# Kernel optimization log

Measured on AMD Instinct MI355X. Metric: run time of the kernel, lower is better.

Reference implementation:

```python
import jax, jax.numpy as jnp
import numpy as np

K_DIM = 1024
HEADS = 16
D_K = K_DIM // HEADS


def setup_inputs() -> dict:
    key = jax.random.key(0)
    ks = jax.random.split(key, 6)
    b, t, k = 4, 1024, K_DIM
    scale = 1.0 / np.sqrt(k)
    return {
        "x": jax.random.normal(ks[0], (b, t, k), dtype=jnp.float32),
        "Wq": jax.random.normal(ks[1], (k, k), dtype=jnp.float32) * scale,
        "Wk": jax.random.normal(ks[2], (k, k), dtype=jnp.float32) * scale,
        "Wv": jax.random.normal(ks[3], (k, k), dtype=jnp.float32) * scale,
        "Wo": jax.random.normal(ks[4], (k, k), dtype=jnp.float32) * scale,
        "bo": jax.random.normal(ks[5], (k,), dtype=jnp.float32) * 0.01,
    }


def reference(x, Wq, Wk, Wv, Wo, bo):
    b, t, k = x.shape
    h, d_k = HEADS, D_K
    # Linear(k,k) applies x @ W.T; project then split heads -> [b, h, t, d_k]
    Q = (x @ Wq.T).reshape(b, t, h, d_k).transpose(0, 2, 1, 3)
    Kh = (x @ Wk.T).reshape(b, t, h, d_k).transpose(0, 2, 1, 3)
    V = (x @ Wv.T).reshape(b, t, h, d_k).transpose(0, 2, 1, 3)
    scores = jnp.einsum("bhqd,bhkd->bhqk", Q, Kh) / jnp.sqrt(jnp.float32(d_k))
    attn = jax.nn.softmax(scores, axis=-1)
    out = jnp.einsum("bhqk,bhkd->bhqd", attn, V)
    out = out.transpose(0, 2, 1, 3).reshape(b, t, k)
    return out @ Wo.T + bo
```

## Files before the change

kernel.cpp:

```cpp
#include <hip/hip_runtime.h>
#include <hip/hip_bf16.h>

typedef __attribute__((ext_vector_type(4))) float f32x4;
typedef __attribute__((ext_vector_type(8))) short short8;

#define B_   4
#define T_   1024
#define H_   16
#define DK_  64
#define KDIM 1024

#define QSCALE 0.18033688011112042f

__device__ __forceinline__ unsigned short f2bf(float f){
  union { float f; unsigned int u; } a; a.f = f;
  unsigned int u = a.u;
  return (unsigned short)((u + 0x7FFFu + ((u >> 16) & 1u)) >> 16);
}

__device__ __forceinline__ unsigned short f2bf_rn(float f){
  union { __hip_bfloat16 h; unsigned short u; } cv;
  cv.h = __float2bfloat16(f);
  return cv.u;
}

__device__ __forceinline__ void gload16(const void* g, void* l){
  __builtin_amdgcn_global_load_lds(
      (const __attribute__((address_space(1))) unsigned int*)g,
      (__attribute__((address_space(3))) unsigned int*)l,
      16, 0, 0);
}

template<int N> __device__ __forceinline__ void wait_vmcnt(){
  if constexpr (N == 0)      asm volatile("s_waitcnt vmcnt(0)" ::: "memory");
  else if constexpr (N == 4) asm volatile("s_waitcnt vmcnt(4)" ::: "memory");
  else if constexpr (N == 6) asm volatile("s_waitcnt vmcnt(6)" ::: "memory");
}

__global__ __launch_bounds__(256) void convert5(
    const float* __restrict__ x,  const float* __restrict__ wq,
    const float* __restrict__ wk, const float* __restrict__ wv,
    const float* __restrict__ wo,
    short* __restrict__ xb,  short* __restrict__ wqb,
    short* __restrict__ wkb, short* __restrict__ wvb, short* __restrict__ wob)
{
  int i = blockIdx.x * 256 + threadIdx.x;
  const float* s; short* d; int off;
  if (i < (1 << 20)) { s = x; d = xb; off = i; }
  else {
    int j = i - (1 << 20);
    int w = j >> 18;
    off = j & ((1 << 18) - 1);
    s = (w == 0) ? wq : (w == 1) ? wk : (w == 2) ? wv : wo;
    d = (w == 0) ? wqb : (w == 1) ? wkb : (w == 2) ? wvb : wob;
  }
  float4 v = ((const float4*)s)[off];
  ushort4 o;
  o.x = f2bf(v.x); o.y = f2bf(v.y); o.z = f2bf(v.z); o.w = f2bf(v.w);
  ((ushort4*)d)[off] = o;
}

template<int BM, int BN>
__device__ __forceinline__ void stage_range(
    const short* __restrict__ A, const short* __restrict__ W,
    int m0, int n0, int kt, int lo, int hi,
    short* Asb, short* Bsb, int wv, int lane)
{
  constexpr int LA = BM / 64, LB = BN / 64;
  const int r8 = lane >> 3;
  const int c8 = ((lane & 7) * 8) ^ (r8 * 8);
#pragma unroll
  for (int i = lo; i < hi; ++i) {
    if (i < LA) {
      const int r = (wv * LA + i) * 8 + r8;
      gload16(A + (size_t)(m0 + r) * KDIM + kt * 64 + c8, Asb + (wv * LA + i) * 512);
    } else {
      const int ib = i - LA;
      const int r = (wv * LB + ib) * 8 + r8;
      gload16(W + (size_t)(n0 + r) * KDIM + kt * 64 + c8, Bsb + (wv * LB + ib) * 512);
    }
  }
}

template<int BM, int BN>
__device__ __forceinline__ void gemm8_core(
    const short* __restrict__ A, const short* __restrict__ W,
    int m0, int n0, short* As, short* Bs,
    f32x4 acc[BM / 64][BN / 32])
{
  constexpr int M_REP = BM / 64, N_REP = BN / 32;
  constexpr int LA = BM / 64, LB = BN / 64, L = LA + LB;
  constexpr int NKT = 16;
  const int tid = threadIdx.x;
  const int wv = tid >> 6, lane = tid & 63;
  const int lr = lane & 15, lq = lane >> 4;
  const int wm = wv >> 1, wn = wv & 1;
  const int arow = wm * (BM / 4);
  const int brow = wn * (BN / 2);
  const int swz = (lr & 7) << 3;

#pragma unroll
  for (int m = 0; m < M_REP; ++m)
#pragma unroll
    for (int n = 0; n < N_REP; ++n) acc[m][n] = (f32x4){0.f, 0.f, 0.f, 0.f};

  stage_range<BM, BN>(A, W, m0, n0, 0, 0, L, As,           Bs,           wv, lane);
  stage_range<BM, BN>(A, W, m0, n0, 1, 0, L, As + BM * 64, Bs + BN * 64, wv, lane);

  int buf = 0;
  for (int kt = 0; kt < NKT; ++kt) {
    if (kt < NKT - 1) wait_vmcnt<L>(); else wait_vmcnt<0>();
    __builtin_amdgcn_s_barrier();
    const short* Ab = As + buf * (BM * 64);
    const short* Bb = Bs + buf * (BN * 64);
    const int sb = (buf >= 1) ? buf - 1 : 2;
    short* Asb = As + sb * (BM * 64);
    short* Bsb = Bs + sb * (BN * 64);
#pragma unroll
    for (int kk = 0; kk < 2; ++kk) {
      short8 af[M_REP], bfv[N_REP];
#pragma unroll
      for (int m = 0; m < M_REP; ++m)
        af[m] = *(const short8*)(Ab + (arow + m * 16 + lr) * 64 + ((kk * 32 + lq * 8) ^ swz));
#pragma unroll
      for (int n = 0; n < N_REP; ++n)
        bfv[n] = *(const short8*)(Bb + (brow + n * 16 + lr) * 64 + ((kk * 32 + lq * 8) ^ swz));
      if (kt + 2 < NKT)
        stage_range<BM, BN>(A, W, m0, n0, kt + 2, kk * (L / 2), (kk + 1) * (L / 2),
                            Asb, Bsb, wv, lane);
      __builtin_amdgcn_s_barrier();
      __builtin_amdgcn_s_setprio(1);
#pragma unroll
      for (int m = 0; m < M_REP; ++m)
#pragma unroll
        for (int n = 0; n < N_REP; ++n)
          acc[m][n] = __builtin_amdgcn_mfma_f32_16x16x32_bf16(af[m], bfv[n], acc[m][n], 0, 0, 0);
      __builtin_amdgcn_s_setprio(0);
      __builtin_amdgcn_sched_barrier(0);
      __builtin_amdgcn_s_barrier();
    }
    buf = (buf == 2) ? 0 : buf + 1;
  }
}

__global__ __launch_bounds__(512, 2) void gemm8_qkv(
    const short* __restrict__ xb,
    const short* __restrict__ Wqb, const short* __restrict__ Wkb, const short* __restrict__ Wvb,
    short* __restrict__ Qb, short* __restrict__ Kb, short* __restrict__ VTb)
{
  __shared__ __align__(16) short As[3 * 256 * 64];
  __shared__ __align__(16) short Bs[3 * 128 * 64];
  const int bid = blockIdx.x;
  const int wgid = (bid & 7) * 48 + (bid >> 3);
  const int mx = wgid / 24, nyy = wgid % 24;
  const int wsel = nyy >> 3;
  const int m0 = mx * 256, n0 = (nyy & 7) * 128;
  const short* W = (wsel == 0) ? Wqb : (wsel == 1) ? Wkb : Wvb;

  f32x4 acc[4][4];
  gemm8_core<256, 128>(xb, W, m0, n0, As, Bs, acc);

  const int tid = threadIdx.x, lane = tid & 63, wv = tid >> 6;
  const int lr = lane & 15, lq = lane >> 4, wm = wv >> 1, wn = wv & 1;
  if (wsel < 2) {
    short* O = wsel ? Kb : Qb;
    const float sc = wsel ? 1.0f : QSCALE;
#pragma unroll
    for (int m = 0; m < 4; ++m)
#pragma unroll
      for (int n = 0; n < 4; ++n)
#pragma unroll
        for (int j = 0; j < 4; ++j) {
          int row = m0 + wm * 64 + m * 16 + lq * 4 + j;
          int col = n0 + wn * 64 + n * 16 + lr;
          O[(size_t)row * KDIM + col] = (short)f2bf(acc[m][n][j] * sc);
        }
  } else {
#pragma unroll
    for (int m = 0; m < 4; ++m)
#pragma unroll
      for (int n = 0; n < 4; ++n) {
        int row = m0 + wm * 64 + m * 16 + lq * 4;
        int col = n0 + wn * 64 + n * 16 + lr;
        int b = row >> 10, t = row & 1023, h = col >> 6, d = col & 63;
        ushort4 v;
        v.x = f2bf(acc[m][n][0]); v.y = f2bf(acc[m][n][1]);
        v.z = f2bf(acc[m][n][2]); v.w = f2bf(acc[m][n][3]);
        *(ushort4*)&VTb[(size_t)((b * 16 + h) * 64 + d) * 1024 + t] = v;
      }
  }
}

__global__ __launch_bounds__(512, 2) void gemm8_out(
    const short* __restrict__ AOb, const short* __restrict__ Wob,
    const float* __restrict__ bias, float* __restrict__ out)
{
  __shared__ __align__(16) short As[3 * 128 * 64];
  __shared__ __align__(16) short Bs[3 * 128 * 64];
  const int bid = blockIdx.x;
  const int wgid = (bid & 7) * 32 + (bid >> 3);
  const int mx = wgid >> 3, ny = wgid & 7;
  const int m0 = mx * 128, n0 = ny * 128;

  f32x4 acc[2][4];
  gemm8_core<128, 128>(AOb, Wob, m0, n0, As, Bs, acc);

  const int tid = threadIdx.x, lane = tid & 63, wv = tid >> 6;
  const int lr = lane & 15, lq = lane >> 4, wm = wv >> 1, wn = wv & 1;
#pragma unroll
  for (int m = 0; m < 2; ++m)
#pragma unroll
    for (int n = 0; n < 4; ++n) {
      int col = n0 + wn * 64 + n * 16 + lr;
      float bv = bias[col];
#pragma unroll
      for (int j = 0; j < 4; ++j) {
        int row = m0 + wm * 32 + m * 16 + lq * 4 + j;
        out[(size_t)row * KDIM + col] = acc[m][n][j] + bv;
      }
    }
}

__global__ __launch_bounds__(256) void attn_kern(
    const short* __restrict__ Qb, const short* __restrict__ Kb,
    const short* __restrict__ VTb, short* __restrict__ AOb)
{
  __shared__ __align__(16) short kl[2][64 * 64];
  __shared__ __align__(16) short vl[2][64 * 64];
  __shared__ __align__(16) short pl[4][16 * 64];
  const int bh = blockIdx.y, b = bh >> 4, h = bh & 15;
  const int q0 = blockIdx.x * 64;
  const int tid = threadIdx.x, wv = tid >> 6, lane = tid & 63;
  const int lr = lane & 15, lq = lane >> 4;

  const short* Qrow = Qb + (size_t)(b * T_ + q0 + wv * 16 + lr) * KDIM + h * DK_;
  short8 qf0 = *(const short8*)(Qrow + lq * 8);
  short8 qf1 = *(const short8*)(Qrow + 32 + lq * 8);

  const short* Kbase = Kb + (size_t)(b * T_) * KDIM + h * DK_;
  const short* Vbase = VTb + (size_t)(bh * DK_) * 1024;

  const int srow = tid >> 3, scol = (tid & 7) * 8;

  auto stage = [&](int buf, int kv0) {
#pragma unroll
    for (int p = 0; p < 2; ++p) {
      const int r = p * 32 + srow;
      gload16(Kbase + (size_t)(kv0 + r) * KDIM + (scol ^ ((r & 7) << 3)),
              &kl[buf][p * 2048 + wv * 512]);
    }
#pragma unroll
    for (int p = 0; p < 2; ++p) {
      const int r = p * 32 + srow;
      gload16(Vbase + (size_t)r * 1024 + kv0 + (scol ^ ((r & 7) << 3)),
              &vl[buf][p * 2048 + wv * 512]);
    }
  };

  f32x4 oacc[4];
#pragma unroll
  for (int i = 0; i < 4; ++i) oacc[i] = (f32x4){0.f, 0.f, 0.f, 0.f};
  float m_r = -1e30f, l_r = 0.f;
  const int swq = (lr & 7) << 3;
  short* plw = pl[wv];

  int cur = 0;
  stage(0, 0);
  __syncthreads();

  for (int kt = 0; kt < 16; ++kt) {
    if (kt < 15) stage(cur ^ 1, (kt + 1) * 64);

    f32x4 s[4];
#pragma unroll
    for (int nt = 0; nt < 4; ++nt) {
      const int kr = nt * 16 + lr;
      const int sw = (kr & 7) << 3;
      short8 kf0 = *(const short8*)&kl[cur][kr * 64 + ((lq * 8) ^ sw)];
      short8 kf1 = *(const short8*)&kl[cur][kr * 64 + ((32 + lq * 8) ^ sw)];
      f32x4 z = (f32x4){0.f, 0.f, 0.f, 0.f};
      z = __builtin_amdgcn_mfma_f32_16x16x32_bf16(kf0, qf0, z, 0, 0, 0);
      s[nt] = __builtin_amdgcn_mfma_f32_16x16x32_bf16(kf1, qf1, z, 0, 0, 0);
    }

    float mx;
    {
      float a0 = fmaxf(fmaxf(s[0][0], s[0][1]), fmaxf(s[0][2], s[0][3]));
      float a1 = fmaxf(fmaxf(s[1][0], s[1][1]), fmaxf(s[1][2], s[1][3]));
      float a2 = fmaxf(fmaxf(s[2][0], s[2][1]), fmaxf(s[2][2], s[2][3]));
      float a3 = fmaxf(fmaxf(s[3][0], s[3][1]), fmaxf(s[3][2], s[3][3]));
      mx = fmaxf(fmaxf(a0, a1), fmaxf(a2, a3));
    }
    mx = fmaxf(mx, __shfl_xor(mx, 16));
    mx = fmaxf(mx, __shfl_xor(mx, 32));
    if (!__all(mx <= m_r + 8.f)) {
      const float mn = fmaxf(m_r, mx);
      const float al = exp2f(m_r - mn);
      l_r *= al;
#pragma unroll
      for (int nt = 0; nt < 4; ++nt)
#pragma unroll
        for (int j = 0; j < 4; ++j) oacc[nt][j] *= al;
      m_r = mn;
    }
    float rs = 0.f;
#pragma unroll
    for (int nt = 0; nt < 4; ++nt)
#pragma unroll
      for (int j = 0; j < 4; ++j) {
        float e = exp2f(s[nt][j] - m_r);
        s[nt][j] = e;
        rs += e;
      }
    rs += __shfl_xor(rs, 16);
    rs += __shfl_xor(rs, 32);
    l_r += rs;

#pragma unroll
    for (int nt = 0; nt < 4; ++nt) {
      f32x4 v = s[nt];
      ushort4 u;
      u.x = f2bf_rn(v[0]); u.y = f2bf_rn(v[1]);
      u.z = f2bf_rn(v[2]); u.w = f2bf_rn(v[3]);
      *(ushort4*)&plw[lr * 64 + ((nt * 16 + lq * 4) ^ swq)] = u;
    }
    asm volatile("s_waitcnt lgkmcnt(0)" ::: "memory");
    short8 pf0 = *(const short8*)&plw[lr * 64 + ((lq * 8) ^ swq)];
    short8 pf1 = *(const short8*)&plw[lr * 64 + ((32 + lq * 8) ^ swq)];
#pragma unroll
    for (int ntd = 0; ntd < 4; ++ntd) {
      const int vr = ntd * 16 + lr;
      const int sw = (vr & 7) << 3;
      short8 vf0 = *(const short8*)&vl[cur][vr * 64 + ((lq * 8) ^ sw)];
      short8 vf1 = *(const short8*)&vl[cur][vr * 64 + ((32 + lq * 8) ^ sw)];
      oacc[ntd] = __builtin_amdgcn_mfma_f32_16x16x32_bf16(vf0, pf0, oacc[ntd], 0, 0, 0);
      oacc[ntd] = __builtin_amdgcn_mfma_f32_16x16x32_bf16(vf1, pf1, oacc[ntd], 0, 0, 0);
    }
    __syncthreads();
    cur ^= 1;
  }

  const float inv = 1.0f / l_r;
#pragma unroll
  for (int nt = 0; nt < 4; ++nt) {
    ushort4 u;
    u.x = f2bf_rn(oacc[nt][0] * inv);
    u.y = f2bf_rn(oacc[nt][1] * inv);
    u.z = f2bf_rn(oacc[nt][2] * inv);
    u.w = f2bf_rn(oacc[nt][3] * inv);
    *(ushort4*)&AOb[(size_t)(b * T_ + q0 + wv * 16 + lr) * KDIM + h * DK_ + nt * 16 + lq * 4] = u;
  }
}

extern "C" void kernel_launch(void* const* d_in, const int* in_sizes, int n_in,
                              void* d_out, int out_size, void* d_ws, size_t ws_size,
                              hipStream_t stream) {
  const float* x  = (const float*)d_in[0];
  const float* Wq = (const float*)d_in[1];
  const float* Wk = (const float*)d_in[2];
  const float* Wv = (const float*)d_in[3];
  const float* Wo = (const float*)d_in[4];
  const float* bo = (const float*)d_in[5];

  short* ws = (short*)d_ws;
  short* xb  = ws;
  short* Wqb = ws + 4194304;
  short* Wkb = ws + 5242880;
  short* Wvb = ws + 6291456;
  short* Wob = ws + 7340032;
  short* Qb  = ws + 8388608;
  short* Kb  = ws + 12582912;
  short* VTb = ws + 16777216;
  short* AOb = ws + 20971520;

  convert5<<<8192, 256, 0, stream>>>(x, Wq, Wk, Wv, Wo, xb, Wqb, Wkb, Wvb, Wob);
  gemm8_qkv<<<384, 512, 0, stream>>>(xb, Wqb, Wkb, Wvb, Qb, Kb, VTb);
  attn_kern<<<dim3(16, 64), 256, 0, stream>>>(Qb, Kb, VTb, AOb);
  gemm8_out<<<256, 512, 0, stream>>>(AOb, Wob, bo, (float*)d_out);
}
```

Baseline: 181.8 us.

## Replace 8-wave triple-buffered GEMMs with 4-wave double-buffered 128x128 tiles

```diff
diff --git a/kernel.cpp b/kernel.cpp
--- a/kernel.cpp
+++ b/kernel.cpp
@@ -29,12 +29,6 @@
       (const __attribute__((address_space(1))) unsigned int*)g,
       (__attribute__((address_space(3))) unsigned int*)l,
       16, 0, 0);
-}
-
-template<int N> __device__ __forceinline__ void wait_vmcnt(){
-  if constexpr (N == 0)      asm volatile("s_waitcnt vmcnt(0)" ::: "memory");
-  else if constexpr (N == 4) asm volatile("s_waitcnt vmcnt(4)" ::: "memory");
-  else if constexpr (N == 6) asm volatile("s_waitcnt vmcnt(6)" ::: "memory");
 }
 
 __global__ __launch_bounds__(256) void convert5(
@@ -60,108 +54,83 @@
   ((ushort4*)d)[off] = o;
 }
 
-template<int BM, int BN>
-__device__ __forceinline__ void stage_range(
+__device__ __forceinline__ void gemm2_core(
     const short* __restrict__ A, const short* __restrict__ W,
-    int m0, int n0, int kt, int lo, int hi,
-    short* Asb, short* Bsb, int wv, int lane)
-{
-  constexpr int LA = BM / 64, LB = BN / 64;
+    int m0, int n0, short* As, short* Bs, f32x4 acc[4][4])
+{
+  const int tid = threadIdx.x, wv = tid >> 6, lane = tid & 63;
+  const int lr = lane & 15, lq = lane >> 4;
+  const int wr = wv >> 1, wc = wv & 1;
+  const int swz = (lr & 7) << 3;
   const int r8 = lane >> 3;
   const int c8 = ((lane & 7) * 8) ^ (r8 * 8);
-#pragma unroll
-  for (int i = lo; i < hi; ++i) {
-    if (i < LA) {
-      const int r = (wv * LA + i) * 8 + r8;
-      gload16(A + (size_t)(m0 + r) * KDIM + kt * 64 + c8, Asb + (wv * LA + i) * 512);
-    } else {
-      const int ib = i - LA;
-      const int r = (wv * LB + ib) * 8 + r8;
-      gload16(W + (size_t)(n0 + r) * KDIM + kt * 64 + c8, Bsb + (wv * LB + ib) * 512);
-    }
-  }
-}
-
-template<int BM, int BN>
-__device__ __forceinline__ void gemm8_core(
-    const short* __restrict__ A, const short* __restrict__ W,
-    int m0, int n0, short* As, short* Bs,
-    f32x4 acc[BM / 64][BN / 32])
-{
-  constexpr int M_REP = BM / 64, N_REP = BN / 32;
-  constexpr int LA = BM / 64, LB = BN / 64, L = LA + LB;
-  constexpr int NKT = 16;
-  const int tid = threadIdx.x;
-  const int wv = tid >> 6, lane = tid & 63;
-  const int lr = lane & 15, lq = lane >> 4;
-  const int wm = wv >> 1, wn = wv & 1;
-  const int arow = wm * (BM / 4);
-  const int brow = wn * (BN / 2);
-  const int swz = (lr & 7) << 3;
-
-#pragma unroll
-  for (int m = 0; m < M_REP; ++m)
-#pragma unroll
-    for (int n = 0; n < N_REP; ++n) acc[m][n] = (f32x4){0.f, 0.f, 0.f, 0.f};
-
-  stage_range<BM, BN>(A, W, m0, n0, 0, 0, L, As,           Bs,           wv, lane);
-  stage_range<BM, BN>(A, W, m0, n0, 1, 0, L, As + BM * 64, Bs + BN * 64, wv, lane);
+
+#pragma unroll
+  for (int m = 0; m < 4; ++m)
+#pragma unroll
+    for (int n = 0; n < 4; ++n) acc[m][n] = (f32x4){0.f, 0.f, 0.f, 0.f};
+
+  auto stage = [&](int buf, int kt) {
+    const int k0 = kt * 64;
+#pragma unroll
+    for (int i = 0; i < 4; ++i) {
+      const int r = (wv * 4 + i) * 8 + r8;
+      gload16(A + (size_t)(m0 + r) * KDIM + k0 + c8, As + buf * 8192 + (wv * 4 + i) * 512);
+      gload16(W + (size_t)(n0 + r) * KDIM + k0 + c8, Bs + buf * 8192 + (wv * 4 + i) * 512);
+    }
+  };
+
+  stage(0, 0);
+  asm volatile("s_waitcnt vmcnt(0)" ::: "memory");
+  __builtin_amdgcn_s_barrier();
 
   int buf = 0;
-  for (int kt = 0; kt < NKT; ++kt) {
-    if (kt < NKT - 1) wait_vmcnt<L>(); else wait_vmcnt<0>();
-    __builtin_amdgcn_s_barrier();
-    const short* Ab = As + buf * (BM * 64);
-    const short* Bb = Bs + buf * (BN * 64);
-    const int sb = (buf >= 1) ? buf - 1 : 2;
-    short* Asb = As + sb * (BM * 64);
-    short* Bsb = Bs + sb * (BN * 64);
+  for (int kt = 0; kt < 16; ++kt) {
+    if (kt < 15) stage(buf ^ 1, kt + 1);
+    const short* Ab = As + buf * 8192;
+    const short* Bb = Bs + buf * 8192;
 #pragma unroll
     for (int kk = 0; kk < 2; ++kk) {
-      short8 af[M_REP], bfv[N_REP];
-#pragma unroll
-      for (int m = 0; m < M_REP; ++m)
-        af[m] = *(const short8*)(Ab + (arow + m * 16 + lr) * 64 + ((kk * 32 + lq * 8) ^ swz));
-#pragma unroll
-      for (int n = 0; n < N_REP; ++n)
-        bfv[n] = *(const short8*)(Bb + (brow + n * 16 + lr) * 64 + ((kk * 32 + lq * 8) ^ swz));
-      if (kt + 2 < NKT)
-        stage_range<BM, BN>(A, W, m0, n0, kt + 2, kk * (L / 2), (kk + 1) * (L / 2),
-                            Asb, Bsb, wv, lane);
-      __builtin_amdgcn_s_barrier();
+      short8 af[4], bfv[4];
+#pragma unroll
+      for (int m = 0; m < 4; ++m)
+        af[m] = *(const short8*)(Ab + (wr * 64 + m * 16 + lr) * 64 + ((kk * 32 + lq * 8) ^ swz));
+#pragma unroll
+      for (int n = 0; n < 4; ++n)
+        bfv[n] = *(const short8*)(Bb + (wc * 64 + n * 16 + lr) * 64 + ((kk * 32 + lq * 8) ^ swz));
       __builtin_amdgcn_s_setprio(1);
 #pragma unroll
-      for (int m = 0; m < M_REP; ++m)
-#pragma unroll
-        for (int n = 0; n < N_REP; ++n)
+      for (int m = 0; m < 4; ++m)
+#pragma unroll
+        for (int n = 0; n < 4; ++n)
           acc[m][n] = __builtin_amdgcn_mfma_f32_16x16x32_bf16(af[m], bfv[n], acc[m][n], 0, 0, 0);
       __builtin_amdgcn_s_setprio(0);
-      __builtin_amdgcn_sched_barrier(0);
-      __builtin_amdgcn_s_barrier();
-    }
-    buf = (buf == 2) ? 0 : buf + 1;
-  }
-}
-
-__global__ __launch_bounds__(512, 2) void gemm8_qkv(
+    }
+    asm volatile("s_waitcnt vmcnt(0)" ::: "memory");
+    __builtin_amdgcn_s_barrier();
+    buf ^= 1;
+  }
+}
+
+__global__ __launch_bounds__(256, 2) void gemm2_qkv(
     const short* __restrict__ xb,
     const short* __restrict__ Wqb, const short* __restrict__ Wkb, const short* __restrict__ Wvb,
     short* __restrict__ Qb, short* __restrict__ Kb, short* __restrict__ VTb)
 {
-  __shared__ __align__(16) short As[3 * 256 * 64];
-  __shared__ __align__(16) short Bs[3 * 128 * 64];
+  __shared__ __align__(16) short As[2 * 8192];
+  __shared__ __align__(16) short Bs[2 * 8192];
   const int bid = blockIdx.x;
-  const int wgid = (bid & 7) * 48 + (bid >> 3);
-  const int mx = wgid / 24, nyy = wgid % 24;
-  const int wsel = nyy >> 3;
-  const int m0 = mx * 256, n0 = (nyy & 7) * 128;
+  const int wgid = (bid & 7) * 96 + (bid >> 3);
+  const int mx = wgid / 24, inner = wgid % 24;
+  const int wsel = inner >> 3;
+  const int m0 = mx * 128, n0 = (inner & 7) * 128;
   const short* W = (wsel == 0) ? Wqb : (wsel == 1) ? Wkb : Wvb;
 
   f32x4 acc[4][4];
-  gemm8_core<256, 128>(xb, W, m0, n0, As, Bs, acc);
+  gemm2_core(xb, W, m0, n0, As, Bs, acc);
 
   const int tid = threadIdx.x, lane = tid & 63, wv = tid >> 6;
-  const int lr = lane & 15, lq = lane >> 4, wm = wv >> 1, wn = wv & 1;
+  const int lr = lane & 15, lq = lane >> 4, wr = wv >> 1, wc = wv & 1;
   if (wsel < 2) {
     short* O = wsel ? Kb : Qb;
     const float sc = wsel ? 1.0f : QSCALE;
@@ -171,8 +140,8 @@
       for (int n = 0; n < 4; ++n)
 #pragma unroll
         for (int j = 0; j < 4; ++j) {
-          int row = m0 + wm * 64 + m * 16 + lq * 4 + j;
-          int col = n0 + wn * 64 + n * 16 + lr;
+          int row = m0 + wr * 64 + m * 16 + lq * 4 + j;
+          int col = n0 + wc * 64 + n * 16 + lr;
           O[(size_t)row * KDIM + col] = (short)f2bf(acc[m][n][j] * sc);
         }
   } else {
@@ -180,8 +149,8 @@
     for (int m = 0; m < 4; ++m)
 #pragma unroll
       for (int n = 0; n < 4; ++n) {
-        int row = m0 + wm * 64 + m * 16 + lq * 4;
-        int col = n0 + wn * 64 + n * 16 + lr;
+        int row = m0 + wr * 64 + m * 16 + lq * 4;
+        int col = n0 + wc * 64 + n * 16 + lr;
         int b = row >> 10, t = row & 1023, h = col >> 6, d = col & 63;
         ushort4 v;
         v.x = f2bf(acc[m][n][0]); v.y = f2bf(acc[m][n][1]);
@@ -191,31 +160,31 @@
   }
 }
 
-__global__ __launch_bounds__(512, 2) void gemm8_out(
+__global__ __launch_bounds__(256, 2) void gemm2_out(
     const short* __restrict__ AOb, const short* __restrict__ Wob,
     const float* __restrict__ bias, float* __restrict__ out)
 {
-  __shared__ __align__(16) short As[3 * 128 * 64];
-  __shared__ __align__(16) short Bs[3 * 128 * 64];
+  __shared__ __align__(16) short As[2 * 8192];
+  __shared__ __align__(16) short Bs[2 * 8192];
   const int bid = blockIdx.x;
   const int wgid = (bid & 7) * 32 + (bid >> 3);
   const int mx = wgid >> 3, ny = wgid & 7;
   const int m0 = mx * 128, n0 = ny * 128;
 
-  f32x4 acc[2][4];
-  gemm8_core<128, 128>(AOb, Wob, m0, n0, As, Bs, acc);
+  f32x4 acc[4][4];
+  gemm2_core(AOb, Wob, m0, n0, As, Bs, acc);
 
   const int tid = threadIdx.x, lane = tid & 63, wv = tid >> 6;
-  const int lr = lane & 15, lq = lane >> 4, wm = wv >> 1, wn = wv & 1;
-#pragma unroll
-  for (int m = 0; m < 2; ++m)
+  const int lr = lane & 15, lq = lane >> 4, wr = wv >> 1, wc = wv & 1;
+#pragma unroll
+  for (int m = 0; m < 4; ++m)
 #pragma unroll
     for (int n = 0; n < 4; ++n) {
-      int col = n0 + wn * 64 + n * 16 + lr;
+      int col = n0 + wc * 64 + n * 16 + lr;
       float bv = bias[col];
 #pragma unroll
       for (int j = 0; j < 4; ++j) {
-        int row = m0 + wm * 32 + m * 16 + lq * 4 + j;
+        int row = m0 + wr * 64 + m * 16 + lq * 4 + j;
         out[(size_t)row * KDIM + col] = acc[m][n][j] + bv;
       }
     }
@@ -228,8 +197,10 @@
   __shared__ __align__(16) short kl[2][64 * 64];
   __shared__ __align__(16) short vl[2][64 * 64];
   __shared__ __align__(16) short pl[4][16 * 64];
-  const int bh = blockIdx.y, b = bh >> 4, h = bh & 15;
-  const int q0 = blockIdx.x * 64;
+  const int flat = blockIdx.y * 16 + blockIdx.x;
+  const int wg = (flat & 7) * 128 + (flat >> 3);
+  const int bh = wg >> 4, b = bh >> 4, h = bh & 15;
+  const int q0 = (wg & 15) * 64;
   const int tid = threadIdx.x, wv = tid >> 6, lane = tid & 63;
   const int lr = lane & 15, lq = lane >> 4;
 
@@ -374,7 +345,7 @@
   short* AOb = ws + 20971520;
 
   convert5<<<8192, 256, 0, stream>>>(x, Wq, Wk, Wv, Wo, xb, Wqb, Wkb, Wvb, Wob);
-  gemm8_qkv<<<384, 512, 0, stream>>>(xb, Wqb, Wkb, Wvb, Qb, Kb, VTb);
+  gemm2_qkv<<<768, 256, 0, stream>>>(xb, Wqb, Wkb, Wvb, Qb, Kb, VTb);
   attn_kern<<<dim3(16, 64), 256, 0, stream>>>(Qb, Kb, VTb, AOb);
-  gemm8_out<<<256, 512, 0, stream>>>(AOb, Wob, bo, (float*)d_out);
-}
+  gemm2_out<<<256, 256, 0, stream>>>(AOb, Wob, bo, (float*)d_out);
+}
```

Measured after the change: 186.9 us. +2.8%, slower.
